# Kernel tuning notes

Measured on AMD Instinct MI355X. Metric: run time of the kernel, lower is better.

## Reference

```python
import jax, jax.numpy as jnp
import numpy as np
from jax import lax

DN = ('NCHW', 'OIHW', 'NCHW')

def _conv(x, w, b, stride, pad):
    y = lax.conv_general_dilated(x, w, (stride, stride), ((pad, pad), (pad, pad)),
                                 dimension_numbers=DN)
    return y + b[None, :, None, None]

def _convT(x, w, b):
    # torch ConvTranspose2d(k=4, s=2, p=1); w: (C_in, C_out, 4, 4)
    wt = jnp.transpose(jnp.flip(w, (2, 3)), (1, 0, 2, 3))  # (C_out, C_in, 4, 4)
    y = lax.conv_general_dilated(x, wt, (1, 1), ((2, 2), (2, 2)),
                                 lhs_dilation=(2, 2), dimension_numbers=DN)
    return y + b[None, :, None, None]

def setup_inputs() -> dict:
    key = jax.random.key(0)
    ks = jax.random.split(key, 20)
    s = 0.05
    inp = {
        'x':   jax.random.normal(ks[0], (8, 1, 256, 256), jnp.float32),
        'ew1': jax.random.normal(ks[1], (64, 1, 3, 3), jnp.float32) * s,
        'eb1': jnp.zeros((64,), jnp.float32),
        'ew2': jax.random.normal(ks[2], (128, 64, 3, 3), jnp.float32) * s,
        'eb2': jnp.zeros((128,), jnp.float32),
        'ew3': jax.random.normal(ks[3], (256, 128, 3, 3), jnp.float32) * s,
        'eb3': jnp.zeros((256,), jnp.float32),
        'ew4': jax.random.normal(ks[4], (256, 256, 1, 1), jnp.float32) * s,
        'eb4': jnp.zeros((256,), jnp.float32),
        # torch init: uniform(-1/K, 1/K) with K=1024
        'codebook': jax.random.uniform(ks[5], (1024, 256), jnp.float32,
                                       minval=-1.0 / 1024, maxval=1.0 / 1024),
        'dw1': jax.random.normal(ks[6], (256, 256, 1, 1), jnp.float32) * s,
        'db1': jnp.zeros((256,), jnp.float32),
        'dw2': jax.random.normal(ks[7], (256, 128, 4, 4), jnp.float32) * s,
        'db2': jnp.zeros((128,), jnp.float32),
        'dw3': jax.random.normal(ks[8], (128, 64, 4, 4), jnp.float32) * s,
        'db3': jnp.zeros((64,), jnp.float32),
        'dw4': jax.random.normal(ks[9], (1, 64, 3, 3), jnp.float32) * s,
        'db4': jnp.zeros((1,), jnp.float32),
        'scale_idx': 2,
    }
    return inp

def reference(x, ew1, eb1, ew2, eb2, ew3, eb3, ew4, eb4, codebook,
              dw1, db1, dw2, db2, dw3, db3, dw4, db4, scale_idx):
    # ---- encoder (scale_idx=2: 1->64->128->256->embedding_dim) ----
    h = jax.nn.relu(_conv(x, ew1, eb1, 1, 1))        # [B,64,256,256]
    h = jax.nn.relu(_conv(h, ew2, eb2, 2, 1))        # [B,128,128,128]
    h = jax.nn.relu(_conv(h, ew3, eb3, 2, 1))        # [B,256,64,64]
    z = _conv(h, ew4, eb4, 1, 0)                     # [B,D,64,64]
    # ---- vector quantization ----
    B, D, H, W = z.shape
    flat = jnp.transpose(z, (0, 2, 3, 1)).reshape(-1, D)        # [N,D]
    dist = (jnp.sum(flat * flat, axis=1, keepdims=True)
            + jnp.sum(codebook * codebook, axis=1)
            - 2.0 * flat @ codebook.T)                          # [N,K]
    idx = jnp.argmin(dist, axis=1)                              # [N]
    quantized = codebook[idx].reshape(B, H, W, D)               # gather == onehot@codebook
    z_q = jnp.transpose(quantized, (0, 3, 1, 2))                # [B,D,H,W]
    indices = idx.reshape(B, H, W)
    # ---- decoder ----
    d = jax.nn.relu(_conv(z_q, dw1, db1, 1, 0))      # [B,256,64,64]
    d = jax.nn.relu(_convT(d, dw2, db2))             # [B,128,128,128]
    d = jax.nn.relu(_convT(d, dw3, db3))             # [B,64,256,256]
    recon = jax.nn.sigmoid(_conv(d, dw4, db4, 1, 1)) # [B,1,256,256]
    return recon, z_q, indices
```

## Files before the change

### kernel.cpp

```cpp
#include <hip/hip_runtime.h>
#include <hip/hip_bf16.h>
#include <math.h>


#define NB 8

typedef short v8s __attribute__((ext_vector_type(8)));
typedef float v4f __attribute__((ext_vector_type(4)));

__device__ __forceinline__ float sumsq128(const float* __restrict__ p, int stride) {
  float r[8];
#pragma unroll
  for (int j = 0; j < 8; ++j) {
    float v = p[(size_t)j * stride];
    r[j] = __fmul_rn(v, v);
  }
  for (int i = 8; i < 128; i += 8) {
#pragma unroll
    for (int j = 0; j < 8; ++j) {
      float v = p[(size_t)(i + j) * stride];
      r[j] = __fadd_rn(r[j], __fmul_rn(v, v));
    }
  }
  return __fadd_rn(__fadd_rn(__fadd_rn(r[0], r[1]), __fadd_rn(r[2], r[3])),
                   __fadd_rn(__fadd_rn(r[4], r[5]), __fadd_rn(r[6], r[7])));
}
__device__ __forceinline__ float sumsq256(const float* __restrict__ p, int stride) {
  return __fadd_rn(sumsq128(p, stride), sumsq128(p + (size_t)128 * stride, stride));
}

__global__ __launch_bounds__(256) void k_conv1(const float* __restrict__ x,
                                               const float* __restrict__ w,
                                               const float* __restrict__ bias,
                                               float* __restrict__ out) {
  int n = blockIdx.z;
  int px = blockIdx.x * 256 + threadIdx.x;
  int y = px >> 8, xx = px & 255;
  const float* xin = x + (size_t)n * 65536;
  float v[9];
#pragma unroll
  for (int dy = 0; dy < 3; ++dy)
#pragma unroll
    for (int dx = 0; dx < 3; ++dx) {
      int iy = y + dy - 1, ix = xx + dx - 1;
      v[dy * 3 + dx] = (iy >= 0 && iy < 256 && ix >= 0 && ix < 256) ? xin[iy * 256 + ix] : 0.f;
    }
  float* o = out + (size_t)n * 64 * 65536 + px;
  for (int co = 0; co < 64; ++co) {
    float acc = bias[co];
#pragma unroll
    for (int k = 0; k < 9; ++k) acc += v[k] * w[co * 9 + k];
    o[(size_t)co * 65536] = fmaxf(acc, 0.f);
  }
}

template <int CI, int IH>
__global__ __launch_bounds__(256) void k_conv3s2(const float* __restrict__ in,
                                                 const float* __restrict__ w,
                                                 const float* __restrict__ bias,
                                                 float* __restrict__ out, int CO) {
  const int OH = IH / 2;
  const int TILES_X = OH / 16;
  const int RS = 40;
  int n = blockIdx.z;
  int cg = blockIdx.y;
  int tile = blockIdx.x;
  int OY0 = (tile / TILES_X) * 16, OX0 = (tile % TILES_X) * 16;
  int ty = threadIdx.x >> 4, tx = threadIdx.x & 15;
  __shared__ float sm[2][33 * RS];
  float acc[32];
#pragma unroll
  for (int c = 0; c < 32; ++c) acc[c] = 0.f;
  int iy0 = 2 * OY0 - 1, ix0 = 2 * OX0 - 1;
  const float* inb = in + (size_t)n * CI * IH * IH;

  for (int t = threadIdx.x; t < 2 * 33 * RS; t += 256) (&sm[0][0])[t] = 0.f;

  int goff[5], loff[5];
  unsigned vmask = 0;
#pragma unroll
  for (int i = 0; i < 5; ++i) {
    int t = threadIdx.x + 256 * i;
    if (t < 33 * 33) {
      int r = t / 33, c = t - r * 33;
      int iy = iy0 + r, ix = ix0 + c;
      if (iy >= 0 && iy < IH && ix >= 0 && ix < IH) {
        vmask |= 1u << i;
        goff[i] = iy * IH + ix;
        loff[i] = r * RS + (c >> 1) + (c & 1) * 17;
      }
    }
  }
  __syncthreads();

  auto stage = [&](int buf, int ci) {
    const float* ip = inb + (size_t)ci * IH * IH;
    float* dst = sm[buf];
#pragma unroll
    for (int i = 0; i < 5; ++i)
      if (vmask & (1u << i)) dst[loff[i]] = ip[goff[i]];
  };
  stage(0, 0);
  for (int ci = 0; ci < CI; ++ci) {
    int buf = ci & 1;
    __syncthreads();
    if (ci + 1 < CI) stage(buf ^ 1, ci + 1);
    float v[9];
#pragma unroll
    for (int dy = 0; dy < 3; ++dy)
#pragma unroll
      for (int dx = 0; dx < 3; ++dx)
        v[dy * 3 + dx] = sm[buf][(2 * ty + dy) * RS + (dx & 1) * 17 + tx + (dx >> 1)];
    const float* wp = w + ((size_t)(cg * 32) * CI + ci) * 9;
#pragma unroll
    for (int c = 0; c < 32; ++c) {
#pragma unroll
      for (int k = 0; k < 9; ++k) acc[c] += v[k] * wp[(size_t)c * CI * 9 + k];
    }
  }
  int oy = OY0 + ty, ox = OX0 + tx;
  float* ob = out + (((size_t)n * CO + cg * 32) * OH + oy) * OH + ox;
#pragma unroll
  for (int c = 0; c < 32; ++c) {
    float r = acc[c] + bias[cg * 32 + c];
    ob[(size_t)c * OH * OH] = fmaxf(r, 0.f);
  }
}

__global__ __launch_bounds__(256) void k_conv1x1(const float* __restrict__ in,
                                                 const float* __restrict__ w,
                                                 const float* __restrict__ bias,
                                                 float* __restrict__ out, int CI, int CO,
                                                 int HW) {
  int n = blockIdx.z;
  int cg = blockIdx.y;
  int px = blockIdx.x * 256 + threadIdx.x;
  __shared__ float sm[16][256];
  const float* inb = in + (size_t)n * CI * HW;
  float acc[8];
#pragma unroll
  for (int c = 0; c < 8; ++c) acc[c] = 0.f;
  for (int c0 = 0; c0 < CI; c0 += 16) {
#pragma unroll
    for (int i = 0; i < 16; ++i) sm[i][threadIdx.x] = inb[(size_t)(c0 + i) * HW + px];
    __syncthreads();
    const float* wb = w + (size_t)(cg * 8) * CI + c0;
#pragma unroll
    for (int i = 0; i < 16; ++i) {
      float r = sm[i][threadIdx.x];
#pragma unroll
      for (int c = 0; c < 8; ++c) acc[c] += r * wb[(size_t)c * CI + i];
    }
    __syncthreads();
  }
#pragma unroll
  for (int c = 0; c < 8; ++c) {
    float r = acc[c] + bias[cg * 8 + c];
    out[((size_t)n * CO + cg * 8 + c) * HW + px] = r;
  }
}

__global__ __launch_bounds__(256) void k_conv1x1_bf(const __hip_bfloat16* __restrict__ in,
                                                    const float* __restrict__ w,
                                                    const float* __restrict__ bias,
                                                    __hip_bfloat16* __restrict__ out,
                                                    int CI, int CO, int HW) {
  int n = blockIdx.z;
  int cg = blockIdx.y;
  int px = blockIdx.x * 256 + threadIdx.x;
  __shared__ float sm[16][256];
  const __hip_bfloat16* inb = in + (size_t)n * CI * HW;
  float acc[8];
#pragma unroll
  for (int c = 0; c < 8; ++c) acc[c] = 0.f;
  for (int c0 = 0; c0 < CI; c0 += 16) {
#pragma unroll
    for (int i = 0; i < 16; ++i)
      sm[i][threadIdx.x] = __bfloat162float(inb[(size_t)(c0 + i) * HW + px]);
    __syncthreads();
    const float* wb = w + (size_t)(cg * 8) * CI + c0;
#pragma unroll
    for (int i = 0; i < 16; ++i) {
      float r = sm[i][threadIdx.x];
#pragma unroll
      for (int c = 0; c < 8; ++c) acc[c] += r * wb[(size_t)c * CI + i];
    }
    __syncthreads();
  }
#pragma unroll
  for (int c = 0; c < 8; ++c) {
    float r = fmaxf(acc[c] + bias[cg * 8 + c], 0.f);
    out[((size_t)n * CO + cg * 8 + c) * HW + px] = __float2bfloat16(r);
  }
}

__global__ __launch_bounds__(256) void k_cnorm(const float* __restrict__ cb,
                                               float* __restrict__ cn) {
  int j = blockIdx.x * 256 + threadIdx.x;
  if (j < 1024) cn[j] = sumsq256(cb + (size_t)j * 256, 1);
}

__global__ __launch_bounds__(256) void k_xnorm(const float* __restrict__ z,
                                               float* __restrict__ xn) {
  int t = blockIdx.x * 256 + threadIdx.x;
  int n = t >> 12, yx = t & 4095;
  xn[t] = sumsq256(z + (size_t)n * 256 * 4096 + yx, 4096);
}

__global__ __launch_bounds__(256) void k_vq(const float* __restrict__ z,
                                            const float* __restrict__ cb,
                                            const float* __restrict__ cn,
                                            const float* __restrict__ xn,
                                            int* __restrict__ idx,
                                            float* __restrict__ idxf) {
  __shared__ __align__(16) float zt[64][68];
  __shared__ float ct[64][65];
  __shared__ float cnt[64];
  __shared__ float xnt[64];
  __shared__ float rbest[64][17];
  __shared__ int ribest[64][17];
  int tid = threadIdx.x;
  int pq = tid & 15;
  int cq = tid >> 4;
  int p0 = blockIdx.x * 64;
  int n = p0 >> 12;
  int yx0 = p0 & 4095;
  const float* zb = z + (size_t)n * 256 * 4096 + yx0;
  if (tid < 64) xnt[tid] = xn[p0 + tid];
  float best[4] = {3.0e38f, 3.0e38f, 3.0e38f, 3.0e38f};
  int bidx[4] = {0, 0, 0, 0};
  for (int c0 = 0; c0 < 1024; c0 += 64) {
    float acc[4][4];
#pragma unroll
    for (int a = 0; a < 4; ++a)
#pragma unroll
      for (int b = 0; b < 4; ++b) acc[a][b] = 0.f;
    for (int k0 = 0; k0 < 256; k0 += 64) {
      __syncthreads();
      for (int t = tid; t < 4096; t += 256) {
        int r = t >> 6, c = t & 63;
        zt[r][c] = zb[(size_t)(k0 + r) * 4096 + c];
      }
      for (int t = tid; t < 4096; t += 256) {
        int c = t >> 6, r = t & 63;
        ct[c][r] = cb[(size_t)(c0 + c) * 256 + k0 + r];
      }
      if (k0 == 0 && tid < 64) cnt[tid] = cn[c0 + tid];
      __syncthreads();
#pragma unroll 8
      for (int k = 0; k < 64; ++k) {
        const float4 zz = *reinterpret_cast<const float4*>(&zt[k][pq * 4]);
#pragma unroll
        for (int j = 0; j < 4; ++j) {
          float cv = ct[cq * 4 + j][k];
          acc[0][j] += zz.x * cv;
          acc[1][j] += zz.y * cv;
          acc[2][j] += zz.z * cv;
          acc[3][j] += zz.w * cv;
        }
      }
    }
#pragma unroll
    for (int pi = 0; pi < 4; ++pi) {
      float xnp = xnt[pq * 4 + pi];
#pragma unroll
      for (int j = 0; j < 4; ++j) {
        float A = __fadd_rn(xnp, cnt[cq * 4 + j]);
        float d = __fsub_rn(A, __fmul_rn(2.0f, acc[pi][j]));
        if (d < best[pi]) {
          best[pi] = d;
          bidx[pi] = c0 + cq * 4 + j;
        }
      }
    }
  }
  __syncthreads();
#pragma unroll
  for (int pi = 0; pi < 4; ++pi) {
    rbest[pq * 4 + pi][cq] = best[pi];
    ribest[pq * 4 + pi][cq] = bidx[pi];
  }
  __syncthreads();
  if (tid < 64) {
    float bv = rbest[tid][0];
    int bj = ribest[tid][0];
    for (int g = 1; g < 16; ++g) {
      float v = rbest[tid][g];
      int j2 = ribest[tid][g];
      if (v < bv || (v == bv && j2 < bj)) { bv = v; bj = j2; }
    }
    idx[p0 + tid] = bj;
    idxf[p0 + tid] = (float)bj;
  }
}

__global__ __launch_bounds__(256) void k_gather(const int* __restrict__ idx,
                                                const float* __restrict__ cb,
                                                float* __restrict__ zq,
                                                __hip_bfloat16* __restrict__ zqbf) {
  size_t t = (size_t)blockIdx.x * 256 + threadIdx.x;
  int yx = (int)(t & 4095);
  int d = (int)((t >> 12) & 255);
  int n = (int)(t >> 20);
  int p = (n << 12) | yx;
  float v = cb[(size_t)idx[p] * 256 + d];
  zq[t] = v;
  zqbf[t] = __float2bfloat16(v);
}

__global__ __launch_bounds__(256) void k_wconv(const float* __restrict__ w,
                                               __hip_bfloat16* __restrict__ wA,
                                               int CI, int CO) {
  int t = blockIdx.x * 256 + threadIdx.x;
  int total = 4 * CO * CI * 4;
  if (t >= total) return;
  int tap = t & 3;
  int q = t >> 2;
  int ci = q % CI;
  int pc = q / CI;
  int co = pc % CO;
  int par = pc / CO;
  int a = tap >> 1, b = tap & 1, ry = par >> 1, rx = par & 1;
  float v = w[((size_t)ci * CO + co) * 16 + (3 - ry - 2 * a) * 4 + (3 - rx - 2 * b)];
  wA[t] = __float2bfloat16(v);
}

template <int CI, int IH, int CO>
__global__ __launch_bounds__(256) void k_convTmfma(const __hip_bfloat16* __restrict__ in,
                                                   const __hip_bfloat16* __restrict__ wA,
                                                   const float* __restrict__ bias,
                                                   __hip_bfloat16* __restrict__ out) {
  const int OH = 2 * IH;
  const int NT = IH / 32;
  int n = blockIdx.z;
  int co0 = blockIdx.y * 64;
  int m = blockIdx.x / NT;
  int n0x = (blockIdx.x % NT) * 32;
  int tid = threadIdx.x;
  int w = tid >> 6, lane = tid & 63, fr = lane & 15, kg = lane >> 4;

  __shared__ __align__(16) ushort Wt[4][64][40];
  __shared__ __align__(16) ushort Bt[4][32][40];
  __shared__ ushort patch[8][3][36];

  v4f acc[4][2];
#pragma unroll
  for (int p = 0; p < 4; ++p)
#pragma unroll
    for (int h = 0; h < 2; ++h) acc[p][h] = (v4f){0.f, 0.f, 0.f, 0.f};

  const ushort* inb = (const ushort*)in + (size_t)n * CI * IH * IH;
  const ushort* wab = (const ushort*)wA;

  for (int t = tid; t < 8 * 3 * 36; t += 256) (&patch[0][0][0])[t] = 0;

  int pgoff[4], ploff[4];
  unsigned pmask = 0;
#pragma unroll
  for (int i = 0; i < 4; ++i) {
    int t = tid + 256 * i;
    if (t < 816) {
      int ci = t / 102;
      int rem = t - ci * 102;
      int r = rem / 34;
      int c = rem - r * 34;
      int iy = m - 1 + r, ix = n0x - 1 + c;
      if (iy >= 0 && iy < IH && ix >= 0 && ix < IH) {
        pmask |= 1u << i;
        pgoff[i] = (ci * IH + iy) * IH + ix;
        ploff[i] = (ci * 3 + r) * 36 + c;
      }
    }
  }

  for (int ci0 = 0; ci0 < CI; ci0 += 8) {
    __syncthreads();
    {
      const ushort* ip = inb + (size_t)ci0 * IH * IH;
      ushort* pb = &patch[0][0][0];
#pragma unroll
      for (int i = 0; i < 4; ++i)
        if (pmask & (1u << i)) pb[ploff[i]] = ip[pgoff[i]];
    }
#pragma unroll
    for (int i = 0; i < 4; ++i) {
      int u = tid + 256 * i;
      int kgg = u & 3, co = (u >> 2) & 63, par = u >> 8;
      const uint4 v =
          *(const uint4*)(wab + (((size_t)par * CO + co0 + co) * CI + ci0) * 4 + kgg * 8);
      *(uint4*)&Wt[par][co][kgg * 8] = v;
    }
    __syncthreads();
    {
      int pr = tid >> 1;
      int px0 = (tid & 1) * 16;
      int par = pr >> 5, k = pr & 31;
      int ci = k >> 2, a = (k >> 1) & 1, b = k & 1, ry = par >> 1, rx = par & 1;
      const ushort* src = &patch[ci][ry + a][px0 + rx + b];
      ushort* dst = &Bt[par][px0][k];
#pragma unroll
      for (int p = 0; p < 16; ++p) dst[p * 40] = src[p];
    }
    __syncthreads();
#pragma unroll
    for (int par = 0; par < 4; ++par) {
      v8s af = *(const v8s*)&Wt[par][w * 16 + fr][kg * 8];
      v8s b0 = *(const v8s*)&Bt[par][fr][kg * 8];
      v8s b1 = *(const v8s*)&Bt[par][16 + fr][kg * 8];
      acc[par][0] = __builtin_amdgcn_mfma_f32_16x16x32_bf16(af, b0, acc[par][0], 0, 0, 0);
      acc[par][1] = __builtin_amdgcn_mfma_f32_16x16x32_bf16(af, b1, acc[par][1], 0, 0, 0);
    }
  }
  __hip_bfloat16* ob = out + (size_t)n * CO * OH * OH;
#pragma unroll
  for (int par = 0; par < 4; ++par) {
    int ry = par >> 1, rx = par & 1;
    int oy = 2 * m + ry;
#pragma unroll
    for (int h = 0; h < 2; ++h) {
      int ox = 2 * (n0x + h * 16 + fr) + rx;
#pragma unroll
      for (int r = 0; r < 4; ++r) {
        int co = co0 + w * 16 + kg * 4 + r;
        float val = acc[par][h][r] + bias[co];
        val = fmaxf(val, 0.f);
        ob[((size_t)co * OH + oy) * OH + ox] = __float2bfloat16(val);
      }
    }
  }
}

__global__ __launch_bounds__(256) void k_conv_out(const __hip_bfloat16* __restrict__ in,
                                                  const float* __restrict__ w,
                                                  const float* __restrict__ bias,
                                                  float* __restrict__ out) {
  int n = blockIdx.z;
  int tile = blockIdx.x;
  int TY0 = (tile / 16) * 16, TX0 = (tile % 16) * 16;
  int ty = threadIdx.x >> 4, tx = threadIdx.x & 15;
  __shared__ float sm[2][18 * 18];
  float acc = bias[0];
  const __hip_bfloat16* inb = in + (size_t)n * 64 * 65536;
  int goff[2], loff[2];
  unsigned vmask = 0;
#pragma unroll
  for (int i = 0; i < 2; ++i) {
    int t = threadIdx.x + 256 * i;
    if (t < 324) {
      int r = t / 18, c = t - r * 18;
      int iy = TY0 - 1 + r, ix = TX0 - 1 + c;
      if (iy >= 0 && iy < 256 && ix >= 0 && ix < 256) {
        vmask |= 1u << i;
        goff[i] = iy * 256 + ix;
        loff[i] = t;
      }
    }
  }
  for (int t = threadIdx.x; t < 2 * 324; t += 256) (&sm[0][0])[t] = 0.f;
  __syncthreads();
  auto stage = [&](int buf, int ci) {
    const __hip_bfloat16* ip = inb + (size_t)ci * 65536;
    float* dst = sm[buf];
#pragma unroll
    for (int i = 0; i < 2; ++i)
      if (vmask & (1u << i)) dst[loff[i]] = __bfloat162float(ip[goff[i]]);
  };
  stage(0, 0);
  for (int ci = 0; ci < 64; ++ci) {
    int buf = ci & 1;
    __syncthreads();
    if (ci + 1 < 64) stage(buf ^ 1, ci + 1);
    const float* wp = w + ci * 9;
#pragma unroll
    for (int dy = 0; dy < 3; ++dy)
#pragma unroll
      for (int dx = 0; dx < 3; ++dx) acc += sm[buf][(ty + dy) * 18 + tx + dx] * wp[dy * 3 + dx];
  }
  out[(size_t)n * 65536 + (TY0 + ty) * 256 + TX0 + tx] = 1.f / (1.f + expf(-acc));
}

extern "C" void kernel_launch(void* const* d_in, const int* in_sizes, int n_in,
                              void* d_out, int out_size, void* d_ws, size_t ws_size,
                              hipStream_t stream) {
  const float* x = (const float*)d_in[0];
  const float* ew1 = (const float*)d_in[1];
  const float* eb1 = (const float*)d_in[2];
  const float* ew2 = (const float*)d_in[3];
  const float* eb2 = (const float*)d_in[4];
  const float* ew3 = (const float*)d_in[5];
  const float* eb3 = (const float*)d_in[6];
  const float* ew4 = (const float*)d_in[7];
  const float* eb4 = (const float*)d_in[8];
  const float* cb = (const float*)d_in[9];
  const float* dw1 = (const float*)d_in[10];
  const float* db1 = (const float*)d_in[11];
  const float* dw2 = (const float*)d_in[12];
  const float* db2 = (const float*)d_in[13];
  const float* dw3 = (const float*)d_in[14];
  const float* db3 = (const float*)d_in[15];
  const float* dw4 = (const float*)d_in[16];
  const float* db4 = (const float*)d_in[17];

  float* ws = (float*)d_ws;
  float* A = ws;
  float* Bb = ws + 33554432;
  float* Cc = ws + 50331648;
  float* cn = A + 16777216;
  float* xn = A + 16778240;
  int* idx = (int*)(A + 16811008);
  __hip_bfloat16* zqbf = (__hip_bfloat16*)(A + 20971520);
  __hip_bfloat16* wbfA2 = (__hip_bfloat16*)(A + 25165824);
  __hip_bfloat16* wbfA3 = (__hip_bfloat16*)(A + 25427968);
  __hip_bfloat16* d1bf = (__hip_bfloat16*)Cc;
  __hip_bfloat16* d2bf = (__hip_bfloat16*)Bb;
  __hip_bfloat16* d3bf = (__hip_bfloat16*)A;

  float* recon = (float*)d_out;
  float* zq = recon + 524288;
  float* idxf = zq + 8388608;

  k_conv1<<<dim3(256, 1, NB), 256, 0, stream>>>(x, ew1, eb1, A);
  k_conv3s2<64, 256><<<dim3(64, 4, NB), 256, 0, stream>>>(A, ew2, eb2, Bb, 128);
  k_conv3s2<128, 128><<<dim3(16, 8, NB), 256, 0, stream>>>(Bb, ew3, eb3, Cc, 256);
  k_conv1x1<<<dim3(16, 32, NB), 256, 0, stream>>>(Cc, ew4, eb4, A, 256, 256, 4096);
  k_wconv<<<2048, 256, 0, stream>>>(dw2, wbfA2, 256, 128);
  k_wconv<<<512, 256, 0, stream>>>(dw3, wbfA3, 128, 64);
  k_cnorm<<<4, 256, 0, stream>>>(cb, cn);
  k_xnorm<<<128, 256, 0, stream>>>(A, xn);
  k_vq<<<512, 256, 0, stream>>>(A, cb, cn, xn, idx, idxf);
  k_gather<<<32768, 256, 0, stream>>>(idx, cb, zq, zqbf);
  k_conv1x1_bf<<<dim3(16, 32, NB), 256, 0, stream>>>(zqbf, dw1, db1, d1bf, 256, 256, 4096);
  k_convTmfma<256, 64, 128><<<dim3(128, 2, NB), 256, 0, stream>>>(d1bf, wbfA2, db2, d2bf);
  k_convTmfma<128, 128, 64><<<dim3(512, 1, NB), 256, 0, stream>>>(d2bf, wbfA3, db3, d3bf);
  k_conv_out<<<dim3(256, 1, NB), 256, 0, stream>>>(d3bf, dw4, db4, recon);
}
```

Measured before the change: 1.990 ms.

## Fuse first two encoder convs and move decoder 1x1 conv to bf16 MFMA

Merges conv1 (1->64, 3x3) into the stride-2 conv2 kernel: each thread recomputes the 3x3 neighborhood of conv1 activations from a 5x5 input patch on the fly, so the 64x256x256 fp32 intermediate is never written to or read from memory. It also replaces the scalar fp32 decoder 1x1 conv with a bf16 MFMA GEMM kernel, using a weight conversion kernel and an LDS transpose of the input tile. The fusion trades memory traffic for roughly 9x redundant conv1 arithmetic per output and high register use (32 accumulators plus 25 inputs). The bf16 weights add a small rounding change.

```diff
diff --git a/kernel.cpp b/kernel.cpp
--- a/kernel.cpp
+++ b/kernel.cpp
@@ -29,28 +29,77 @@
   return __fadd_rn(sumsq128(p, stride), sumsq128(p + (size_t)128 * stride, stride));
 }
 
-__global__ __launch_bounds__(256) void k_conv1(const float* __restrict__ x,
-                                               const float* __restrict__ w,
-                                               const float* __restrict__ bias,
-                                               float* __restrict__ out) {
+__global__ __launch_bounds__(256) void k_conv12(const float* __restrict__ x,
+                                                const float* __restrict__ ew1,
+                                                const float* __restrict__ eb1,
+                                                const float* __restrict__ ew2,
+                                                const float* __restrict__ bias2,
+                                                float* __restrict__ out) {
+  const int IH = 256;
+  const int OH = 128;
+  const int TILES_X = OH / 16;
   int n = blockIdx.z;
-  int px = blockIdx.x * 256 + threadIdx.x;
-  int y = px >> 8, xx = px & 255;
-  const float* xin = x + (size_t)n * 65536;
-  float v[9];
+  int cg = blockIdx.y;
+  int tile = blockIdx.x;
+  int OY0 = (tile / TILES_X) * 16, OX0 = (tile % TILES_X) * 16;
+  int ty = threadIdx.x >> 4, tx = threadIdx.x & 15;
+  int oy = OY0 + ty, ox = OX0 + tx;
+
+  const float* xin = x + (size_t)n * IH * IH;
+  float xv[5][5];
+#pragma unroll
+  for (int a = 0; a < 5; ++a)
+#pragma unroll
+    for (int b = 0; b < 5; ++b) {
+      int iy = 2 * oy - 2 + a, ix = 2 * ox - 2 + b;
+      xv[a][b] = (iy >= 0 && iy < IH && ix >= 0 && ix < IH) ? xin[iy * IH + ix] : 0.f;
+    }
+
+  unsigned hmask = 0;
 #pragma unroll
   for (int dy = 0; dy < 3; ++dy)
 #pragma unroll
     for (int dx = 0; dx < 3; ++dx) {
-      int iy = y + dy - 1, ix = xx + dx - 1;
-      v[dy * 3 + dx] = (iy >= 0 && iy < 256 && ix >= 0 && ix < 256) ? xin[iy * 256 + ix] : 0.f;
-    }
-  float* o = out + (size_t)n * 64 * 65536 + px;
-  for (int co = 0; co < 64; ++co) {
-    float acc = bias[co];
-#pragma unroll
-    for (int k = 0; k < 9; ++k) acc += v[k] * w[co * 9 + k];
-    o[(size_t)co * 65536] = fmaxf(acc, 0.f);
+      int hy = 2 * oy - 1 + dy, hx = 2 * ox - 1 + dx;
+      if (hy >= 0 && hy < IH && hx >= 0 && hx < IH) hmask |= 1u << (dy * 3 + dx);
+    }
+
+  float acc[32];
+#pragma unroll
+  for (int c = 0; c < 32; ++c) acc[c] = 0.f;
+
+  for (int ci = 0; ci < 64; ++ci) {
+    const float* w1 = ew1 + ci * 9;
+    float b1 = eb1[ci];
+    float v[9];
+#pragma unroll
+    for (int dy = 0; dy < 3; ++dy)
+#pragma unroll
+      for (int dx = 0; dx < 3; ++dx) {
+        int k = dy * 3 + dx;
+        if (hmask & (1u << k)) {
+          float h = b1;
+#pragma unroll
+          for (int ey = 0; ey < 3; ++ey)
+#pragma unroll
+            for (int ex = 0; ex < 3; ++ex) h += xv[dy + ey][dx + ex] * w1[ey * 3 + ex];
+          v[k] = fmaxf(h, 0.f);
+        } else {
+          v[k] = 0.f;
+        }
+      }
+    const float* wp = ew2 + ((size_t)(cg * 32) * 64 + ci) * 9;
+#pragma unroll
+    for (int c = 0; c < 32; ++c) {
+#pragma unroll
+      for (int k = 0; k < 9; ++k) acc[c] += v[k] * wp[(size_t)c * 64 * 9 + k];
+    }
+  }
+  float* ob = out + (((size_t)n * 128 + cg * 32) * OH + oy) * OH + ox;
+#pragma unroll
+  for (int c = 0; c < 32; ++c) {
+    float r = acc[c] + bias2[cg * 32 + c];
+    ob[(size_t)c * OH * OH] = fmaxf(r, 0.f);
   }
 }
 
@@ -157,40 +206,6 @@
   for (int c = 0; c < 8; ++c) {
     float r = acc[c] + bias[cg * 8 + c];
     out[((size_t)n * CO + cg * 8 + c) * HW + px] = r;
-  }
-}
-
-__global__ __launch_bounds__(256) void k_conv1x1_bf(const __hip_bfloat16* __restrict__ in,
-                                                    const float* __restrict__ w,
-                                                    const float* __restrict__ bias,
-                                                    __hip_bfloat16* __restrict__ out,
-                                                    int CI, int CO, int HW) {
-  int n = blockIdx.z;
-  int cg = blockIdx.y;
-  int px = blockIdx.x * 256 + threadIdx.x;
-  __shared__ float sm[16][256];
-  const __hip_bfloat16* inb = in + (size_t)n * CI * HW;
-  float acc[8];
-#pragma unroll
-  for (int c = 0; c < 8; ++c) acc[c] = 0.f;
-  for (int c0 = 0; c0 < CI; c0 += 16) {
-#pragma unroll
-    for (int i = 0; i < 16; ++i)
-      sm[i][threadIdx.x] = __bfloat162float(inb[(size_t)(c0 + i) * HW + px]);
-    __syncthreads();
-    const float* wb = w + (size_t)(cg * 8) * CI + c0;
-#pragma unroll
-    for (int i = 0; i < 16; ++i) {
-      float r = sm[i][threadIdx.x];
-#pragma unroll
-      for (int c = 0; c < 8; ++c) acc[c] += r * wb[(size_t)c * CI + i];
-    }
-    __syncthreads();
-  }
-#pragma unroll
-  for (int c = 0; c < 8; ++c) {
-    float r = fmaxf(acc[c] + bias[cg * 8 + c], 0.f);
-    out[((size_t)n * CO + cg * 8 + c) * HW + px] = __float2bfloat16(r);
   }
 }
 
@@ -325,6 +340,68 @@
   wA[t] = __float2bfloat16(v);
 }
 
+__global__ __launch_bounds__(256) void k_wconv1(const float* __restrict__ w,
+                                                __hip_bfloat16* __restrict__ wb) {
+  int t = blockIdx.x * 256 + threadIdx.x;
+  if (t < 65536) wb[t] = __float2bfloat16(w[t]);
+}
+
+__global__ __launch_bounds__(256) void k_d1mfma(const __hip_bfloat16* __restrict__ in,
+                                                const __hip_bfloat16* __restrict__ wb,
+                                                const float* __restrict__ bias,
+                                                __hip_bfloat16* __restrict__ out) {
+  int n = blockIdx.z;
+  int co0 = blockIdx.y * 64;
+  int px0 = blockIdx.x * 64;
+  int tid = threadIdx.x;
+  int w = tid >> 6, lane = tid & 63, fr = lane & 15, kg = lane >> 4;
+
+  __shared__ __align__(16) ushort Wt[64][40];
+  __shared__ __align__(16) ushort Zt[64][40];
+
+  v4f acc[4];
+#pragma unroll
+  for (int q = 0; q < 4; ++q) acc[q] = (v4f){0.f, 0.f, 0.f, 0.f};
+
+  const ushort* inb = (const ushort*)in + (size_t)n * 256 * 4096;
+  const ushort* wab = (const ushort*)wb;
+
+  for (int k0 = 0; k0 < 256; k0 += 32) {
+    __syncthreads();
+    {
+      int co = tid & 63, kgg = tid >> 6;
+      const uint4 v = *(const uint4*)(wab + (size_t)(co0 + co) * 256 + k0 + kgg * 8);
+      *(uint4*)&Wt[co][kgg * 8] = v;
+    }
+    {
+      int ci = tid >> 3, pxg = tid & 7;
+      const ushort* src = inb + (size_t)(k0 + ci) * 4096 + px0 + pxg * 8;
+      uint4 v = *(const uint4*)src;
+      const ushort* vs = (const ushort*)&v;
+#pragma unroll
+      for (int j = 0; j < 8; ++j) Zt[pxg * 8 + j][ci] = vs[j];
+    }
+    __syncthreads();
+    v8s af = *(const v8s*)&Wt[w * 16 + fr][kg * 8];
+#pragma unroll
+    for (int q = 0; q < 4; ++q) {
+      v8s b = *(const v8s*)&Zt[q * 16 + fr][kg * 8];
+      acc[q] = __builtin_amdgcn_mfma_f32_16x16x32_bf16(af, b, acc[q], 0, 0, 0);
+    }
+  }
+  __hip_bfloat16* ob = out + (size_t)n * 256 * 4096;
+#pragma unroll
+  for (int q = 0; q < 4; ++q) {
+    int px = px0 + q * 16 + fr;
+#pragma unroll
+    for (int r = 0; r < 4; ++r) {
+      int co = co0 + w * 16 + kg * 4 + r;
+      float val = fmaxf(acc[q][r] + bias[co], 0.f);
+      ob[(size_t)co * 4096 + px] = __float2bfloat16(val);
+    }
+  }
+}
+
 template <int CI, int IH, int CO>
 __global__ __launch_bounds__(256) void k_convTmfma(const __hip_bfloat16* __restrict__ in,
                                                    const __hip_bfloat16* __restrict__ wA,
@@ -511,6 +588,7 @@
   __hip_bfloat16* zqbf = (__hip_bfloat16*)(A + 20971520);
   __hip_bfloat16* wbfA2 = (__hip_bfloat16*)(A + 25165824);
   __hip_bfloat16* wbfA3 = (__hip_bfloat16*)(A + 25427968);
+  __hip_bfloat16* wbf1 = (__hip_bfloat16*)(A + 25493504);
   __hip_bfloat16* d1bf = (__hip_bfloat16*)Cc;
   __hip_bfloat16* d2bf = (__hip_bfloat16*)Bb;
   __hip_bfloat16* d3bf = (__hip_bfloat16*)A;
@@ -519,17 +597,17 @@
   float* zq = recon + 524288;
   float* idxf = zq + 8388608;
 
-  k_conv1<<<dim3(256, 1, NB), 256, 0, stream>>>(x, ew1, eb1, A);
-  k_conv3s2<64, 256><<<dim3(64, 4, NB), 256, 0, stream>>>(A, ew2, eb2, Bb, 128);
+  k_conv12<<<dim3(64, 4, NB), 256, 0, stream>>>(x, ew1, eb1, ew2, eb2, Bb);
   k_conv3s2<128, 128><<<dim3(16, 8, NB), 256, 0, stream>>>(Bb, ew3, eb3, Cc, 256);
   k_conv1x1<<<dim3(16, 32, NB), 256, 0, stream>>>(Cc, ew4, eb4, A, 256, 256, 4096);
   k_wconv<<<2048, 256, 0, stream>>>(dw2, wbfA2, 256, 128);
   k_wconv<<<512, 256, 0, stream>>>(dw3, wbfA3, 128, 64);
+  k_wconv1<<<256, 256, 0, stream>>>(dw1, wbf1);
   k_cnorm<<<4, 256, 0, stream>>>(cb, cn);
   k_xnorm<<<128, 256, 0, stream>>>(A, xn);
   k_vq<<<512, 256, 0, stream>>>(A, cb, cn, xn, idx, idxf);
   k_gather<<<32768, 256, 0, stream>>>(idx, cb, zq, zqbf);
-  k_conv1x1_bf<<<dim3(16, 32, NB), 256, 0, stream>>>(zqbf, dw1, db1, d1bf, 256, 256, 4096);
+  k_d1mfma<<<dim3(64, 4, NB), 256, 0, stream>>>(zqbf, wbf1, db1, d1bf);
   k_convTmfma<256, 64, 128><<<dim3(128, 2, NB), 256, 0, stream>>>(d1bf, wbfA2, db2, d2bf);
   k_convTmfma<128, 128, 64><<<dim3(512, 1, NB), 256, 0, stream>>>(d2bf, wbfA3, db3, d3bf);
   k_conv_out<<<dim3(256, 1, NB), 256, 0, stream>>>(d3bf, dw4, db4, recon);
```

After: 1.845 ms. -7.3%, faster.
